# Kernel optimization log

Measured on AMD Instinct MI355X. Metric: run time of the kernel, lower is better.

The kernel has to match this reference:

```python
import jax, jax.numpy as jnp
import numpy as np
from jax import lax

B, E, DIN = 16, 1024, 128   # batch, num_edges, link_state_dim
P, D = 2048, 128            # num_paths, path_state_dim


def _topology():
    # deterministic ragged paths: lengths in [4,16], at least one of max length 16
    lengths = 4 + (np.arange(P) % 13)
    idx = np.repeat(np.arange(P), lengths).astype(np.int32)          # path id per entry
    seqs = np.concatenate([np.arange(l) for l in lengths]).astype(np.int32)  # position in path
    paths = np.random.RandomState(0).randint(0, E, size=idx.shape[0]).astype(np.int32)
    return paths, idx, seqs


def setup_inputs() -> dict:
    key = jax.random.key(0)
    ks = jax.random.split(key, 8)
    paths, idx, seqs = _topology()
    s_in = 1.0 / np.sqrt(DIN)
    s_h = 1.0 / np.sqrt(D)
    return dict(
        inputs=jax.random.normal(ks[0], (B, E, DIN), jnp.float32),
        W_in=jax.random.normal(ks[1], (DIN, 3 * D), jnp.float32) * s_in,
        W_rec=jax.random.normal(ks[2], (D, 3 * D), jnp.float32) * s_h,
        b_in=jnp.zeros((3 * D,), jnp.float32),
        b_rec=jnp.zeros((3 * D,), jnp.float32),
        wq=jax.random.normal(ks[3], (D, D), jnp.float32) * s_h,
        wk=jax.random.normal(ks[4], (D, D), jnp.float32) * s_h,
        wv=jax.random.normal(ks[5], (D, D), jnp.float32) * s_h,
        paths=paths, idx=idx, seqs=seqs,
    )


def _forward(inputs, W_in, W_rec, b_in, b_rec, wq, wk, wv, paths, idx, seqs, max_len):
    Bc = inputs.shape[0]
    # --- ragged gather -> dense zero-padded tensor [B, P, max_len, DIN] (tf.gather + scatter_nd) ---
    h_tild = inputs[:, paths]                                  # [B, n_entries, DIN]
    link = jnp.zeros((Bc, P, max_len, DIN), inputs.dtype)
    link = link.at[:, idx, seqs].set(h_tild)
    x = link.reshape(Bc * P, max_len, DIN)                     # [BP, L, DIN]
    # --- GRU over time (keras GRUCell default: reset_after=True, tanh/sigmoid) ---
    xg = jnp.einsum('nld,de->lne', x, W_in) + b_in             # [L, BP, 3D]
    h0 = jnp.zeros((Bc * P, D), inputs.dtype)

    def step(h, xg_t):
        hg = h @ W_rec + b_rec                                 # [BP, 3D]
        xz, xr, xh = jnp.split(xg_t, 3, axis=-1)
        hz, hr, hh = jnp.split(hg, 3, axis=-1)
        z = jax.nn.sigmoid(xz + hz)
        r = jax.nn.sigmoid(xr + hr)
        hc = jnp.tanh(xh + r * hh)
        hn = z * h + (1.0 - z) * hc
        return hn, hn

    last, hs = lax.scan(step, h0, xg)                          # last:[BP,D], hs:[L,BP,D]
    hs = jnp.transpose(hs, (1, 0, 2))                          # [BP, L, D]
    # --- single-query QKV attention (raw scores, no softmax, as in source) ---
    key_ = hs @ wk                                             # [BP, L, D]
    val = hs @ wv                                              # [BP, L, D]
    q = last @ wq                                              # [BP, D]
    att = jnp.einsum('nld,nd->nl', key_, q)                    # [BP, L]
    ctx = jnp.einsum('nl,nld->nd', att, val)                   # [BP, D]
    return ctx.reshape(Bc, P, D)


def reference(inputs, W_in, W_rec, b_in, b_rec, wq, wk, wv, paths, idx, seqs):
    max_len = int(np.max(np.asarray(seqs))) + 1                # static (16)
    return _forward(inputs, W_in, W_rec, b_in, b_rec, wq, wk, wv, paths, idx, seqs, max_len)
```

## Files before the change

### kernel.cpp

```cpp
#include <hip/hip_runtime.h>
#include <hip/hip_bf16.h>
#include <cstddef>

#define P_ 2048
#define B_ 16
#define E_ 1024
#define D_ 128
#define L_ 16
#define TD_ 384

#define NEG_L2E (-1.44269504088896340736f)
#define TWO_L2E (2.88539008177792681472f)

typedef _Float16 f16x2 __attribute__((ext_vector_type(2)));
typedef _Float16 f16x8 __attribute__((ext_vector_type(8)));
typedef float    f32x4 __attribute__((ext_vector_type(4)));

__device__ __forceinline__ unsigned short f2h(float x) {
    _Float16 h = (_Float16)x;
    return __builtin_bit_cast(unsigned short, h);
}
__device__ __forceinline__ unsigned pk2(float a, float b) {
    return __builtin_bit_cast(unsigned, __builtin_amdgcn_cvt_pkrtz(a, b));
}
__device__ __forceinline__ float lo16(unsigned u) {
    return (float)__builtin_bit_cast(f16x2, u)[0];
}
__device__ __forceinline__ float hi16(unsigned u) {
    return (float)__builtin_bit_cast(f16x2, u)[1];
}
__device__ __forceinline__ float ex2(float x) {
#if __has_builtin(__builtin_amdgcn_exp2f)
    return __builtin_amdgcn_exp2f(x);
#else
    return exp2f(x);
#endif
}
__device__ __forceinline__ float dot2w(unsigned hu, unsigned qu, float c) {
#if __has_builtin(__builtin_amdgcn_fdot2)
    typedef __fp16 h2v __attribute__((ext_vector_type(2)));
    return __builtin_amdgcn_fdot2(__builtin_bit_cast(h2v, hu),
                                  __builtin_bit_cast(h2v, qu), c, false);
#else
    f16x2 h = __builtin_bit_cast(f16x2, hu), q = __builtin_bit_cast(f16x2, qu);
    return c + (float)h[0] * (float)q[0] + (float)h[1] * (float)q[1];
#endif
}

__device__ __forceinline__ void wf16(const float* __restrict__ src,
                                     unsigned short* __restrict__ dst, int g, int N,
                                     float sc) {
    int lane = g & 63, kt = (g >> 6) & 3, tile = g >> 8;
    int k0 = kt * 32 + (lane >> 4) * 8;
    int c = tile * 16 + (lane & 15);
#pragma unroll
    for (int j = 0; j < 8; ++j)
        dst[(size_t)g * 8 + j] = f2h(src[(size_t)(k0 + j) * N + c] * sc);
}

__device__ __forceinline__ void* hp(void* base, int t, int s, int boff) {
    return (char*)base + ((t * 16 + s) << 8) + (boff ^ ((s & 7) << 4));
}
__device__ __forceinline__ const void* hpc(const void* base, int t, int s, int boff) {
    return (const char*)base + ((t * 16 + s) << 8) + (boff ^ ((s & 7) << 4));
}

__global__ __launch_bounds__(256) void k_prep(const float* __restrict__ W_in,
                                              const float* __restrict__ wq,
                                              const float* __restrict__ wk,
                                              unsigned short* __restrict__ WfI,
                                              unsigned short* __restrict__ Mf) {
    __shared__ float wk_lds[128 * 129];
    __shared__ float wq_row2[2][128];
    int blk = blockIdx.x, tid = threadIdx.x;
    if (blk < 24) {
        int gg = blk * 256 + tid;
        wf16(W_in, WfI, gg, TD_, ((gg >> 8) < 16) ? NEG_L2E : TWO_L2E);
        return;
    }
    int j0 = (blk - 24) * 2;
    int d = tid & 127, half = tid >> 7;
    for (int r = half * 64; r < half * 64 + 64; ++r)
        wk_lds[r * 129 + d] = wk[r * 128 + d];
    wq_row2[half][d] = wq[(j0 + half) * 128 + d];
    __syncthreads();
    float acc = 0.f;
    for (int k = 0; k < 128; ++k) acc += wq_row2[half][k] * wk_lds[d * 129 + k];
    {
        int r = j0 + half;
        int tile = d >> 4, kt = r >> 5;
        int ln = ((r >> 3) & 3) * 16 + (d & 15), jj = r & 7;
        Mf[((size_t)(tile * 4 + kt) * 64 + ln) * 8 + jj] = f2h(acc);
    }
}

__global__ __launch_bounds__(256) void k_G(const float* __restrict__ inputs,
                                           const unsigned short* __restrict__ WfI,
                                           const float* __restrict__ b_in,
                                           const float* __restrict__ b_rec,
                                           unsigned short* __restrict__ G2,
                                           const float* __restrict__ W_rec,
                                           const float* __restrict__ wv,
                                           const int* __restrict__ paths,
                                           int* __restrict__ pt,
                                           unsigned short* __restrict__ WfR,
                                           unsigned short* __restrict__ wvf) {
    if (blockIdx.x >= 1024) {
        int tb = blockIdx.x - 1024, tid = threadIdx.x;
        if (tb < 128) {
            int gid = tb * 256 + tid;
            int p = gid >> 4, s = gid & 15;
            int c = p / 13, r = p - c * 13;
            int len = 4 + r;
            int off = 4 * p + 78 * c + (r * (r - 1)) / 2;
            pt[gid] = (s < len) ? paths[off + s] : E_;
        } else if (tb < 152) {
            int gg = (tb - 128) * 256 + tid;
            wf16(W_rec, WfR, gg, TD_, ((gg >> 8) < 16) ? NEG_L2E : TWO_L2E);
        } else if (tb < 160) {
            wf16(wv, wvf, (tb - 152) * 256 + tid, 128, 1.f);
        } else {
            for (int i = tid; i < 2048; i += 256) {
                int bx = i >> 7, cc = i & 127;
                size_t base = ((size_t)(bx * (E_ + 1) + E_) * 128 + cc) * 4;
                G2[base]     = f2h((b_in[cc] + b_rec[cc]) * NEG_L2E);
                G2[base + 1] = f2h((b_in[128 + cc] + b_rec[128 + cc]) * NEG_L2E);
                G2[base + 2] = f2h(b_in[256 + cc] * TWO_L2E);
                G2[base + 3] = 0;
            }
        }
        return;
    }
    __shared__ __align__(16) unsigned short a_lds[16][136];
    __shared__ __align__(16) unsigned short g_lds[16][128][4];
    int tid = threadIdx.x, w = tid >> 6, L = tid & 63;
    int l15 = L & 15, q = L >> 4;
    int row0 = blockIdx.x * 16;
    int badd = row0 >> 10;
    {
        int r = tid >> 4, c = (tid & 15) * 8;
        const float4* p = (const float4*)(inputs + (size_t)(row0 + r) * 128 + c);
        float4 v0 = p[0], v1 = p[1];
        uint4 st;
        st.x = pk2(v0.x, v0.y); st.y = pk2(v0.z, v0.w);
        st.z = pk2(v1.x, v1.y); st.w = pk2(v1.z, v1.w);
        *(uint4*)&a_lds[r][c] = st;
    }
    __syncthreads();
    f16x8 af[4];
#pragma unroll
    for (int kt = 0; kt < 4; ++kt)
        af[kt] = *(const f16x8*)&a_lds[l15][kt * 32 + q * 8];
#pragma unroll
    for (int ct = 0; ct < 6; ++ct) {
        int tl = 6 * w + ct;
        f32x4 acc = (f32x4){0.f, 0.f, 0.f, 0.f};
#pragma unroll
        for (int kt = 0; kt < 4; ++kt)
            acc = __builtin_amdgcn_mfma_f32_16x16x32_f16(
                af[kt], *(const f16x8*)(WfI + (size_t)((tl * 4 + kt) * 64 + L) * 8), acc, 0, 0, 0);
        int g  = tl >> 3;
        int dd = (tl & 7) * 16 + l15;
        float sg  = (g < 2) ? NEG_L2E : TWO_L2E;
        float bia = (b_in[tl * 16 + l15] + (g < 2 ? b_rec[tl * 16 + l15] : 0.f)) * sg;
#pragma unroll
        for (int j = 0; j < 4; ++j) {
            int r = q * 4 + j;
            g_lds[r][dd][g] = f2h(acc[j] + bia);
        }
    }
    __syncthreads();
    {
        const uint4* src = (const uint4*)g_lds;
        uint4* dst = (uint4*)(G2 + (size_t)(row0 + badd) * 512);
#pragma unroll
        for (int i = 0; i < 4; ++i) dst[tid + 256 * i] = src[tid + 256 * i];
    }
}

__global__ __launch_bounds__(512, 2) void k_rec(const unsigned short* __restrict__ WfR,
                                                const float* __restrict__ b_rec,
                                                const unsigned short* __restrict__ G2,
                                                const int* __restrict__ pt,
                                                const unsigned short* __restrict__ Mf,
                                                const unsigned short* __restrict__ wvf,
                                                float* __restrict__ out) {
    __shared__ __align__(16) unsigned short hsl[16][16][128];
    __shared__ __align__(16) unsigned short qkb[16][136];
    __shared__ __align__(16) unsigned short svb[16][136];
    __shared__ float attp[2][16][16];
    __shared__ int ofs_lds[16][16];

    int tid = threadIdx.x, w = tid >> 6, L = tid & 63;
    int l15 = L & 15, q = L >> 4;
    int c0 = 16 * w + 4 * q;
    int n0 = blockIdx.x * 16;
    int b  = n0 >> 11;
    int p0 = n0 & (P_ - 1);
    int bb = b * (E_ + 1);

    f16x8 afw[3][4];
#pragma unroll
    for (int g = 0; g < 3; ++g)
#pragma unroll
        for (int kt = 0; kt < 4; ++kt)
            afw[g][kt] = *(const f16x8*)(WfR + (size_t)(((g * 8 + w) * 4 + kt) * 64 + L) * 8);

    if (tid < 256)
        ofs_lds[tid >> 4][tid & 15] = (bb + pt[p0 * L_ + tid]) << 10;

    f32x4 rh4;
#pragma unroll
    for (int j = 0; j < 4; ++j) rh4[j] = b_rec[256 + c0 + j] * TWO_L2E;
    float h_reg[4] = {0.f, 0.f, 0.f, 0.f};
    __syncthreads();

    const char* g2c = (const char*)G2 + (size_t)c0 * 8;
    int ocur = ofs_lds[l15][0];
    uint4 cur0 = *(const uint4*)(g2c + ocur);
    uint4 cur1 = *(const uint4*)(g2c + ocur + 16);

#pragma unroll
    for (int t = 0; t < L_; ++t) {
        uint4 nx0 = cur0, nx1 = cur1;
        int onext = ocur;
        if (t < 15) {
            onext = ofs_lds[l15][t + 1];
            const char* gp = g2c + onext;
            nx0 = *(const uint4*)(gp);
            nx1 = *(const uint4*)(gp + 16);
        }

        float xh[4];
        f32x4 acc[3];
        acc[0][0] = lo16(cur0.x); acc[0][1] = lo16(cur0.z);
        acc[0][2] = lo16(cur1.x); acc[0][3] = lo16(cur1.z);
        acc[1][0] = hi16(cur0.x); acc[1][1] = hi16(cur0.z);
        acc[1][2] = hi16(cur1.x); acc[1][3] = hi16(cur1.z);
        xh[0] = lo16(cur0.y); xh[1] = lo16(cur0.w);
        xh[2] = lo16(cur1.y); xh[3] = lo16(cur1.w);
        acc[2] = rh4;

        if (t > 0) {
            f16x8 hf[4];
#pragma unroll
            for (int kt = 0; kt < 4; ++kt)
                hf[kt] = *(const f16x8*)hpc(hsl, t - 1, l15, kt * 64 + q * 16);
#pragma unroll
            for (int g = 0; g < 3; ++g)
#pragma unroll
                for (int kt = 0; kt < 4; ++kt)
                    acc[g] = __builtin_amdgcn_mfma_f32_16x16x32_f16(afw[g][kt], hf[kt], acc[g], 0, 0, 0);
        }

        float z4[4], r4[4];
#pragma unroll
        for (int j = 0; j < 4; ++j) {
            z4[j] = __builtin_amdgcn_rcpf(1.f + ex2(acc[0][j]));
            r4[j] = __builtin_amdgcn_rcpf(1.f + ex2(acc[1][j]));
        }
        float hn[4];
#pragma unroll
        for (int j = 0; j < 4; ++j) {
            float pre = fminf(xh[j] + r4[j] * acc[2][j], 30.f);
            float hc  = 1.f - 2.f * __builtin_amdgcn_rcpf(1.f + ex2(pre));
            hn[j] = hc + z4[j] * (h_reg[j] - hc);
            h_reg[j] = hn[j];
        }
        uint2 st;
        st.x = pk2(hn[0], hn[1]); st.y = pk2(hn[2], hn[3]);
        *(uint2*)hp(hsl, t, l15, c0 * 2) = st;
        cur0 = nx0; cur1 = nx1; ocur = onext;

        __builtin_amdgcn_wave_barrier();
        __builtin_amdgcn_s_waitcnt(0xC07F);
        __builtin_amdgcn_s_barrier();
        __builtin_amdgcn_wave_barrier();
    }

    {
        f16x8 hf[4];
#pragma unroll
        for (int kt = 0; kt < 4; ++kt)
            hf[kt] = *(const f16x8*)hpc(hsl, 15, l15, kt * 64 + q * 16);
        f32x4 a = (f32x4){0.f, 0.f, 0.f, 0.f};
#pragma unroll
        for (int kt = 0; kt < 4; ++kt)
            a = __builtin_amdgcn_mfma_f32_16x16x32_f16(
                *(const f16x8*)(Mf + (size_t)((w * 4 + kt) * 64 + L) * 8), hf[kt], a, 0, 0, 0);
        uint2 st;
        st.x = pk2(a[0], a[1]); st.y = pk2(a[2], a[3]);
        *(uint2*)&qkb[l15][c0] = st;
    }
    __syncthreads();

    {
        int s = tid & 15, l = (tid >> 4) & 15, half = tid >> 8;
        const uint4* qr = (const uint4*)&qkb[s][half * 64];
        float a = 0.f;
#pragma unroll
        for (int k8 = 0; k8 < 8; ++k8) {
            uint4 hh = *(const uint4*)hpc(hsl, l, s, half * 128 + k8 * 16);
            uint4 qq = qr[k8];
            a = dot2w(hh.x, qq.x, a); a = dot2w(hh.y, qq.y, a);
            a = dot2w(hh.z, qq.z, a); a = dot2w(hh.w, qq.w, a);
        }
        attp[half][s][l] = a;
    }
    __syncthreads();

    {
        int s = tid >> 5, d0 = (tid & 31) * 4;
        float v[4] = {0.f, 0.f, 0.f, 0.f};
#pragma unroll
        for (int l = 0; l < 16; ++l) {
            float a = attp[0][s][l] + attp[1][s][l];
            uint2 hu = *(const uint2*)hpc(hsl, l, s, d0 * 2);
            v[0] += a * lo16(hu.x); v[1] += a * hi16(hu.x);
            v[2] += a * lo16(hu.y); v[3] += a * hi16(hu.y);
        }
        uint2 st;
        st.x = pk2(v[0], v[1]); st.y = pk2(v[2], v[3]);
        *(uint2*)&svb[s][d0] = st;
    }
    __syncthreads();

    {
        f16x8 sf[4];
#pragma unroll
        for (int kt = 0; kt < 4; ++kt)
            sf[kt] = *(const f16x8*)&svb[l15][kt * 32 + q * 8];
        f32x4 a = (f32x4){0.f, 0.f, 0.f, 0.f};
#pragma unroll
        for (int kt = 0; kt < 4; ++kt)
            a = __builtin_amdgcn_mfma_f32_16x16x32_f16(
                *(const f16x8*)(wvf + (size_t)((w * 4 + kt) * 64 + L) * 8), sf[kt], a, 0, 0, 0);
        *(f32x4*)&out[(size_t)(n0 + l15) * D_ + c0] = a;
    }
}

extern "C" void kernel_launch(void* const* d_in, const int* in_sizes, int n_in,
                              void* d_out, int out_size, void* d_ws, size_t ws_size,
                              hipStream_t stream) {
    const float* inputs = (const float*)d_in[0];
    const float* W_in   = (const float*)d_in[1];
    const float* W_rec  = (const float*)d_in[2];
    const float* b_in   = (const float*)d_in[3];
    const float* b_rec  = (const float*)d_in[4];
    const float* wq     = (const float*)d_in[5];
    const float* wk     = (const float*)d_in[6];
    const float* wvp    = (const float*)d_in[7];
    const int* paths    = (const int*)d_in[8];

    const size_t off_pt  = 0;
    const size_t off_WfR = off_pt  + (size_t)P_ * L_ * 4;
    const size_t off_WfI = off_WfR + (size_t)24 * 256 * 16;
    const size_t off_Mf  = off_WfI + (size_t)24 * 256 * 16;
    const size_t off_wvf = off_Mf  + (size_t)8 * 256 * 16;
    const size_t off_G2  = off_wvf + (size_t)8 * 256 * 16;
    char* ws = (char*)d_ws;
    int* pt             = (int*)(ws + off_pt);
    unsigned short* WfR = (unsigned short*)(ws + off_WfR);
    unsigned short* WfI = (unsigned short*)(ws + off_WfI);
    unsigned short* Mf  = (unsigned short*)(ws + off_Mf);
    unsigned short* wvf = (unsigned short*)(ws + off_wvf);
    unsigned short* G2  = (unsigned short*)(ws + off_G2);
    float* out = (float*)d_out;

    k_prep<<<dim3(88), dim3(256), 0, stream>>>(W_in, wq, wk, WfI, Mf);
    k_G<<<dim3(1024 + 161), dim3(256), 0, stream>>>(inputs, WfI, b_in, b_rec, G2,
                                                    W_rec, wvp, paths, pt, WfR, wvf);
    k_rec<<<dim3(B_ * P_ / 16), dim3(512), 0, stream>>>(WfR, b_rec, G2, pt,
                                                        Mf, wvf, out);
}
```

Baseline: 175.3 us.

## Raise recurrent kernel occupancy by streaming weights and spilling hidden history to global

The recurrent kernel no longer keeps the W_rec fragments in registers. It reloads them from global/L2 every step, using an opaque zero offset so the compiler cannot hoist the loads. The 16-step hidden-state history moves out of shared memory into a global workspace buffer, leaving only a two-slot rolling buffer in LDS. Launch bounds rise from 2 to 6 blocks per CU. The aim is to hide per-step latency with more resident blocks, at the cost of extra global traffic for weights and hidden states; a fallback to the old kernel is used if the workspace is too small.

```diff
diff --git a/kernel.cpp b/kernel.cpp
--- a/kernel.cpp
+++ b/kernel.cpp
@@ -178,14 +178,15 @@
     }
 }
 
-__global__ __launch_bounds__(512, 2) void k_rec(const unsigned short* __restrict__ WfR,
+__global__ __launch_bounds__(512, 6) void k_rec(const unsigned short* __restrict__ WfR,
                                                 const float* __restrict__ b_rec,
                                                 const unsigned short* __restrict__ G2,
                                                 const int* __restrict__ pt,
                                                 const unsigned short* __restrict__ Mf,
                                                 const unsigned short* __restrict__ wvf,
+                                                unsigned short* __restrict__ Hb,
                                                 float* __restrict__ out) {
-    __shared__ __align__(16) unsigned short hsl[16][16][128];
+    __shared__ __align__(16) unsigned short roll[2][16][128];
     __shared__ __align__(16) unsigned short qkb[16][136];
     __shared__ __align__(16) unsigned short svb[16][136];
     __shared__ float attp[2][16][16];
@@ -198,13 +199,10 @@
     int b  = n0 >> 11;
     int p0 = n0 & (P_ - 1);
     int bb = b * (E_ + 1);
-
-    f16x8 afw[3][4];
-#pragma unroll
-    for (int g = 0; g < 3; ++g)
-#pragma unroll
-        for (int kt = 0; kt < 4; ++kt)
-            afw[g][kt] = *(const f16x8*)(WfR + (size_t)(((g * 8 + w) * 4 + kt) * 64 + L) * 8);
+    unsigned short* hbB = Hb + (size_t)blockIdx.x * (16 * 16 * 128);
+
+    int kzero = 0;
+    asm volatile("" : "+s"(kzero));
 
     if (tid < 256)
         ofs_lds[tid >> 4][tid & 15] = (bb + pt[p0 * L_ + tid]) << 10;
@@ -230,6 +228,7 @@
             nx0 = *(const uint4*)(gp);
             nx1 = *(const uint4*)(gp + 16);
         }
+        const unsigned short* WfRt = WfR + (size_t)(t * kzero);
 
         float xh[4];
         f32x4 acc[3];
@@ -245,12 +244,15 @@
             f16x8 hf[4];
 #pragma unroll
             for (int kt = 0; kt < 4; ++kt)
-                hf[kt] = *(const f16x8*)hpc(hsl, t - 1, l15, kt * 64 + q * 16);
-#pragma unroll
-            for (int g = 0; g < 3; ++g)
+                hf[kt] = *(const f16x8*)hpc(roll, (t - 1) & 1, l15, kt * 64 + q * 16);
+#pragma unroll
+            for (int g = 0; g < 3; ++g) {
+                const f16x8* wp = (const f16x8*)(WfRt + ((size_t)((g * 8 + w) * 4) * 64 + L) * 8);
 #pragma unroll
                 for (int kt = 0; kt < 4; ++kt)
-                    acc[g] = __builtin_amdgcn_mfma_f32_16x16x32_f16(afw[g][kt], hf[kt], acc[g], 0, 0, 0);
+                    acc[g] = __builtin_amdgcn_mfma_f32_16x16x32_f16(
+                        wp[(size_t)kt * 64], hf[kt], acc[g], 0, 0, 0);
+            }
         }
 
         float z4[4], r4[4];
@@ -269,7 +271,8 @@
         }
         uint2 st;
         st.x = pk2(hn[0], hn[1]); st.y = pk2(hn[2], hn[3]);
-        *(uint2*)hp(hsl, t, l15, c0 * 2) = st;
+        *(uint2*)hp(roll, t & 1, l15, c0 * 2) = st;
+        *(uint2*)(hbB + ((size_t)t * 16 + l15) * 128 + c0) = st;
         cur0 = nx0; cur1 = nx1; ocur = onext;
 
         __builtin_amdgcn_wave_barrier();
@@ -282,7 +285,7 @@
         f16x8 hf[4];
 #pragma unroll
         for (int kt = 0; kt < 4; ++kt)
-            hf[kt] = *(const f16x8*)hpc(hsl, 15, l15, kt * 64 + q * 16);
+            hf[kt] = *(const f16x8*)hpc(roll, 1, l15, kt * 64 + q * 16);
         f32x4 a = (f32x4){0.f, 0.f, 0.f, 0.f};
 #pragma unroll
         for (int kt = 0; kt < 4; ++kt)
@@ -296,6 +299,165 @@
 
     {
         int s = tid & 15, l = (tid >> 4) & 15, half = tid >> 8;
+        const uint4* hr = (const uint4*)(hbB + ((size_t)l * 16 + s) * 128 + half * 64);
+        const uint4* qr = (const uint4*)&qkb[s][half * 64];
+        float a = 0.f;
+#pragma unroll
+        for (int k8 = 0; k8 < 8; ++k8) {
+            uint4 hh = hr[k8];
+            uint4 qq = qr[k8];
+            a = dot2w(hh.x, qq.x, a); a = dot2w(hh.y, qq.y, a);
+            a = dot2w(hh.z, qq.z, a); a = dot2w(hh.w, qq.w, a);
+        }
+        attp[half][s][l] = a;
+    }
+    __syncthreads();
+
+    {
+        int s = tid >> 5, d0 = (tid & 31) * 4;
+        float v[4] = {0.f, 0.f, 0.f, 0.f};
+#pragma unroll
+        for (int l = 0; l < 16; ++l) {
+            float a = attp[0][s][l] + attp[1][s][l];
+            uint2 hu = *(const uint2*)(hbB + ((size_t)l * 16 + s) * 128 + d0);
+            v[0] += a * lo16(hu.x); v[1] += a * hi16(hu.x);
+            v[2] += a * lo16(hu.y); v[3] += a * hi16(hu.y);
+        }
+        uint2 st;
+        st.x = pk2(v[0], v[1]); st.y = pk2(v[2], v[3]);
+        *(uint2*)&svb[s][d0] = st;
+    }
+    __syncthreads();
+
+    {
+        f16x8 sf[4];
+#pragma unroll
+        for (int kt = 0; kt < 4; ++kt)
+            sf[kt] = *(const f16x8*)&svb[l15][kt * 32 + q * 8];
+        f32x4 a = (f32x4){0.f, 0.f, 0.f, 0.f};
+#pragma unroll
+        for (int kt = 0; kt < 4; ++kt)
+            a = __builtin_amdgcn_mfma_f32_16x16x32_f16(
+                *(const f16x8*)(wvf + (size_t)((w * 4 + kt) * 64 + L) * 8), sf[kt], a, 0, 0, 0);
+        *(f32x4*)&out[(size_t)(n0 + l15) * D_ + c0] = a;
+    }
+}
+
+__global__ __launch_bounds__(512, 2) void k_rec_f(const unsigned short* __restrict__ WfR,
+                                                  const float* __restrict__ b_rec,
+                                                  const unsigned short* __restrict__ G2,
+                                                  const int* __restrict__ pt,
+                                                  const unsigned short* __restrict__ Mf,
+                                                  const unsigned short* __restrict__ wvf,
+                                                  float* __restrict__ out) {
+    __shared__ __align__(16) unsigned short hsl[16][16][128];
+    __shared__ __align__(16) unsigned short qkb[16][136];
+    __shared__ __align__(16) unsigned short svb[16][136];
+    __shared__ float attp[2][16][16];
+    __shared__ int ofs_lds[16][16];
+
+    int tid = threadIdx.x, w = tid >> 6, L = tid & 63;
+    int l15 = L & 15, q = L >> 4;
+    int c0 = 16 * w + 4 * q;
+    int n0 = blockIdx.x * 16;
+    int b  = n0 >> 11;
+    int p0 = n0 & (P_ - 1);
+    int bb = b * (E_ + 1);
+
+    f16x8 afw[3][4];
+#pragma unroll
+    for (int g = 0; g < 3; ++g)
+#pragma unroll
+        for (int kt = 0; kt < 4; ++kt)
+            afw[g][kt] = *(const f16x8*)(WfR + (size_t)(((g * 8 + w) * 4 + kt) * 64 + L) * 8);
+
+    if (tid < 256)
+        ofs_lds[tid >> 4][tid & 15] = (bb + pt[p0 * L_ + tid]) << 10;
+
+    f32x4 rh4;
+#pragma unroll
+    for (int j = 0; j < 4; ++j) rh4[j] = b_rec[256 + c0 + j] * TWO_L2E;
+    float h_reg[4] = {0.f, 0.f, 0.f, 0.f};
+    __syncthreads();
+
+    const char* g2c = (const char*)G2 + (size_t)c0 * 8;
+    int ocur = ofs_lds[l15][0];
+    uint4 cur0 = *(const uint4*)(g2c + ocur);
+    uint4 cur1 = *(const uint4*)(g2c + ocur + 16);
+
+#pragma unroll
+    for (int t = 0; t < L_; ++t) {
+        uint4 nx0 = cur0, nx1 = cur1;
+        int onext = ocur;
+        if (t < 15) {
+            onext = ofs_lds[l15][t + 1];
+            const char* gp = g2c + onext;
+            nx0 = *(const uint4*)(gp);
+            nx1 = *(const uint4*)(gp + 16);
+        }
+        float xh[4];
+        f32x4 acc[3];
+        acc[0][0] = lo16(cur0.x); acc[0][1] = lo16(cur0.z);
+        acc[0][2] = lo16(cur1.x); acc[0][3] = lo16(cur1.z);
+        acc[1][0] = hi16(cur0.x); acc[1][1] = hi16(cur0.z);
+        acc[1][2] = hi16(cur1.x); acc[1][3] = hi16(cur1.z);
+        xh[0] = lo16(cur0.y); xh[1] = lo16(cur0.w);
+        xh[2] = lo16(cur1.y); xh[3] = lo16(cur1.w);
+        acc[2] = rh4;
+
+        if (t > 0) {
+            f16x8 hf[4];
+#pragma unroll
+            for (int kt = 0; kt < 4; ++kt)
+                hf[kt] = *(const f16x8*)hpc(hsl, t - 1, l15, kt * 64 + q * 16);
+#pragma unroll
+            for (int g = 0; g < 3; ++g)
+#pragma unroll
+                for (int kt = 0; kt < 4; ++kt)
+                    acc[g] = __builtin_amdgcn_mfma_f32_16x16x32_f16(afw[g][kt], hf[kt], acc[g], 0, 0, 0);
+        }
+        float z4[4], r4[4];
+#pragma unroll
+        for (int j = 0; j < 4; ++j) {
+            z4[j] = __builtin_amdgcn_rcpf(1.f + ex2(acc[0][j]));
+            r4[j] = __builtin_amdgcn_rcpf(1.f + ex2(acc[1][j]));
+        }
+        float hn[4];
+#pragma unroll
+        for (int j = 0; j < 4; ++j) {
+            float pre = fminf(xh[j] + r4[j] * acc[2][j], 30.f);
+            float hc  = 1.f - 2.f * __builtin_amdgcn_rcpf(1.f + ex2(pre));
+            hn[j] = hc + z4[j] * (h_reg[j] - hc);
+            h_reg[j] = hn[j];
+        }
+        uint2 st;
+        st.x = pk2(hn[0], hn[1]); st.y = pk2(hn[2], hn[3]);
+        *(uint2*)hp(hsl, t, l15, c0 * 2) = st;
+        cur0 = nx0; cur1 = nx1; ocur = onext;
+
+        __builtin_amdgcn_wave_barrier();
+        __builtin_amdgcn_s_waitcnt(0xC07F);
+        __builtin_amdgcn_s_barrier();
+        __builtin_amdgcn_wave_barrier();
+    }
+
+    {
+        f16x8 hf[4];
+#pragma unroll
+        for (int kt = 0; kt < 4; ++kt)
+            hf[kt] = *(const f16x8*)hpc(hsl, 15, l15, kt * 64 + q * 16);
+        f32x4 a = (f32x4){0.f, 0.f, 0.f, 0.f};
+#pragma unroll
+        for (int kt = 0; kt < 4; ++kt)
+            a = __builtin_amdgcn_mfma_f32_16x16x32_f16(
+                *(const f16x8*)(Mf + (size_t)((w * 4 + kt) * 64 + L) * 8), hf[kt], a, 0, 0, 0);
+        uint2 st;
+        st.x = pk2(a[0], a[1]); st.y = pk2(a[2], a[3]);
+        *(uint2*)&qkb[l15][c0] = st;
+    }
+    __syncthreads();
+    {
+        int s = tid & 15, l = (tid >> 4) & 15, half = tid >> 8;
         const uint4* qr = (const uint4*)&qkb[s][half * 64];
         float a = 0.f;
 #pragma unroll
@@ -308,7 +470,6 @@
         attp[half][s][l] = a;
     }
     __syncthreads();
-
     {
         int s = tid >> 5, d0 = (tid & 31) * 4;
         float v[4] = {0.f, 0.f, 0.f, 0.f};
@@ -324,7 +485,6 @@
         *(uint2*)&svb[s][d0] = st;
     }
     __syncthreads();
-
     {
         f16x8 sf[4];
 #pragma unroll
@@ -358,6 +518,8 @@
     const size_t off_Mf  = off_WfI + (size_t)24 * 256 * 16;
     const size_t off_wvf = off_Mf  + (size_t)8 * 256 * 16;
     const size_t off_G2  = off_wvf + (size_t)8 * 256 * 16;
+    const size_t off_Hb  = off_G2  + (size_t)16 * 1025 * 128 * 4 * 2;
+    const size_t NEED    = off_Hb  + (size_t)2048 * 16 * 16 * 128 * 2;
     char* ws = (char*)d_ws;
     int* pt             = (int*)(ws + off_pt);
     unsigned short* WfR = (unsigned short*)(ws + off_WfR);
@@ -365,11 +527,16 @@
     unsigned short* Mf  = (unsigned short*)(ws + off_Mf);
     unsigned short* wvf = (unsigned short*)(ws + off_wvf);
     unsigned short* G2  = (unsigned short*)(ws + off_G2);
+    unsigned short* Hb  = (unsigned short*)(ws + off_Hb);
     float* out = (float*)d_out;
 
     k_prep<<<dim3(88), dim3(256), 0, stream>>>(W_in, wq, wk, WfI, Mf);
     k_G<<<dim3(1024 + 161), dim3(256), 0, stream>>>(inputs, WfI, b_in, b_rec, G2,
                                                     W_rec, wvp, paths, pt, WfR, wvf);
-    k_rec<<<dim3(B_ * P_ / 16), dim3(512), 0, stream>>>(WfR, b_rec, G2, pt,
-                                                        Mf, wvf, out);
-}
+    if (ws_size >= NEED)
+        k_rec<<<dim3(B_ * P_ / 16), dim3(512), 0, stream>>>(WfR, b_rec, G2, pt,
+                                                            Mf, wvf, Hb, out);
+    else
+        k_rec_f<<<dim3(B_ * P_ / 16), dim3(512), 0, stream>>>(WfR, b_rec, G2, pt,
+                                                              Mf, wvf, out);
+}
```

After: 282.3 us. 61.0% more time.

## Batch reciprocals via product trick, preload offsets, raise k_rec occupancy

Applied to the files above, without the earlier changes.

Replaces the twelve per-element reciprocals in the GRU step with three batched inversions (Montgomery trick, one rcp per four values) to cut transcendental-unit pressure. Per-lane gather offsets are loaded once from LDS into registers instead of being read each step. The launch bound is raised from 2 to 4 blocks per CU, which forces the compiler to use fewer registers and may cause spills given the held weight fragments and the new offset array. The product of four denominators can overflow float when the exponent inputs are large, which risks inf or NaN in the gates.

```diff
diff --git a/kernel.cpp b/kernel.cpp
--- a/kernel.cpp
+++ b/kernel.cpp
@@ -45,6 +45,19 @@
     f16x2 h = __builtin_bit_cast(f16x2, hu), q = __builtin_bit_cast(f16x2, qu);
     return c + (float)h[0] * (float)q[0] + (float)h[1] * (float)q[1];
 #endif
+}
+
+__device__ __forceinline__ void binv4(const float* __restrict__ d, float* __restrict__ o) {
+    float f1 = d[0] * d[1];
+    float f2 = f1 * d[2];
+    float f3 = f2 * d[3];
+    float r  = __builtin_amdgcn_rcpf(f3);
+    o[3] = r * f2;
+    float t  = r * d[3];
+    o[2] = t * f1;
+    float u  = t * d[2];
+    o[1] = u * d[0];
+    o[0] = u * d[1];
 }
 
 __device__ __forceinline__ void wf16(const float* __restrict__ src,
@@ -178,7 +191,7 @@
     }
 }
 
-__global__ __launch_bounds__(512, 2) void k_rec(const unsigned short* __restrict__ WfR,
+__global__ __launch_bounds__(512, 4) void k_rec(const unsigned short* __restrict__ WfR,
                                                 const float* __restrict__ b_rec,
                                                 const unsigned short* __restrict__ G2,
                                                 const int* __restrict__ pt,
@@ -215,18 +228,25 @@
     float h_reg[4] = {0.f, 0.f, 0.f, 0.f};
     __syncthreads();
 
+    int ofs[16];
+    {
+        const uint4* op = (const uint4*)&ofs_lds[l15][0];
+        uint4 o0 = op[0], o1 = op[1], o2 = op[2], o3 = op[3];
+        ofs[0]  = o0.x; ofs[1]  = o0.y; ofs[2]  = o0.z; ofs[3]  = o0.w;
+        ofs[4]  = o1.x; ofs[5]  = o1.y; ofs[6]  = o1.z; ofs[7]  = o1.w;
+        ofs[8]  = o2.x; ofs[9]  = o2.y; ofs[10] = o2.z; ofs[11] = o2.w;
+        ofs[12] = o3.x; ofs[13] = o3.y; ofs[14] = o3.z; ofs[15] = o3.w;
+    }
+
     const char* g2c = (const char*)G2 + (size_t)c0 * 8;
-    int ocur = ofs_lds[l15][0];
-    uint4 cur0 = *(const uint4*)(g2c + ocur);
-    uint4 cur1 = *(const uint4*)(g2c + ocur + 16);
+    uint4 cur0 = *(const uint4*)(g2c + ofs[0]);
+    uint4 cur1 = *(const uint4*)(g2c + ofs[0] + 16);
 
 #pragma unroll
     for (int t = 0; t < L_; ++t) {
         uint4 nx0 = cur0, nx1 = cur1;
-        int onext = ocur;
         if (t < 15) {
-            onext = ofs_lds[l15][t + 1];
-            const char* gp = g2c + onext;
+            const char* gp = g2c + ofs[t + 1];
             nx0 = *(const uint4*)(gp);
             nx1 = *(const uint4*)(gp + 16);
         }
@@ -253,24 +273,32 @@
                     acc[g] = __builtin_amdgcn_mfma_f32_16x16x32_f16(afw[g][kt], hf[kt], acc[g], 0, 0, 0);
         }
 
+        float dz[4], dr[4];
+#pragma unroll
+        for (int j = 0; j < 4; ++j) {
+            dz[j] = 1.f + ex2(acc[0][j]);
+            dr[j] = 1.f + ex2(acc[1][j]);
+        }
         float z4[4], r4[4];
+        binv4(dz, z4);
+        binv4(dr, r4);
+        float dh[4];
+#pragma unroll
+        for (int j = 0; j < 4; ++j)
+            dh[j] = 1.f + ex2(fminf(xh[j] + r4[j] * acc[2][j], 30.f));
+        float y4[4];
+        binv4(dh, y4);
+        float hn[4];
 #pragma unroll
         for (int j = 0; j < 4; ++j) {
-            z4[j] = __builtin_amdgcn_rcpf(1.f + ex2(acc[0][j]));
-            r4[j] = __builtin_amdgcn_rcpf(1.f + ex2(acc[1][j]));
-        }
-        float hn[4];
-#pragma unroll
-        for (int j = 0; j < 4; ++j) {
-            float pre = fminf(xh[j] + r4[j] * acc[2][j], 30.f);
-            float hc  = 1.f - 2.f * __builtin_amdgcn_rcpf(1.f + ex2(pre));
+            float hc = 1.f - 2.f * y4[j];
             hn[j] = hc + z4[j] * (h_reg[j] - hc);
             h_reg[j] = hn[j];
         }
         uint2 st;
         st.x = pk2(hn[0], hn[1]); st.y = pk2(hn[2], hn[3]);
         *(uint2*)hp(hsl, t, l15, c0 * 2) = st;
-        cur0 = nx0; cur1 = nx1; ocur = onext;
+        cur0 = nx0; cur1 = nx1;
 
         __builtin_amdgcn_wave_barrier();
         __builtin_amdgcn_s_waitcnt(0xC07F);
```

New measurement: 172.7 us (median of 2 runs). About the same (-1.5%).
